# Performance work log

Hardware: AMD Instinct MI355X
Metric: run time of the kernel (lower is better)

## Reference

```python
import jax, jax.numpy as jnp
import numpy as np

N_RES = 256
D_PAIR = 128
NUM_HEADS = 16
D_HEAD = 32
D_INNER = NUM_HEADS * D_HEAD  # 512


def setup_inputs() -> dict:
    key = jax.random.key(0)
    ks = jax.random.split(key, 5)
    s_in = 1.0 / np.sqrt(D_PAIR)
    s_out = 1.0 / np.sqrt(D_INNER)
    return {
        "pair_repr": jax.random.normal(ks[0], (N_RES, N_RES, D_PAIR), jnp.float32),
        "Wq": jax.random.normal(ks[1], (D_PAIR, D_INNER), jnp.float32) * s_in,
        "bq": jnp.zeros((D_INNER,), jnp.float32),
        "Wk": jax.random.normal(ks[2], (D_PAIR, D_INNER), jnp.float32) * s_in,
        "bk": jnp.zeros((D_INNER,), jnp.float32),
        "Wv": jax.random.normal(ks[3], (D_PAIR, D_INNER), jnp.float32) * s_in,
        "bv": jnp.zeros((D_INNER,), jnp.float32),
        "Wo": jax.random.normal(ks[4], (D_INNER, D_PAIR), jnp.float32) * s_out,
        "bo": jnp.zeros((D_PAIR,), jnp.float32),
    }


def reference(pair_repr, Wq, bq, Wk, bk, Wv, bv, Wo, bo):
    N = pair_repr.shape[0]
    # Projections -> (N, N, H, Dh)
    q = (pair_repr @ Wq + bq).reshape(N, N, NUM_HEADS, D_HEAD)
    k = (pair_repr @ Wk + bk).reshape(N, N, NUM_HEADS, D_HEAD)
    v = (pair_repr @ Wv + bv).reshape(N, N, NUM_HEADS, D_HEAD)
    # Triangular attention for starting nodes: attend over k index per row i.
    a = jnp.einsum('ijhc,ikhc->ijkh', q, k) / jnp.sqrt(jnp.asarray(D_HEAD, q.dtype))
    # Lower-triangular mask over (j, k), broadcast over (i, h).
    mask = jnp.tril(jnp.ones((N, N), dtype=bool))[None, :, :, None]
    a = jnp.where(mask, a, jnp.asarray(-1e9, a.dtype))
    a = jax.nn.softmax(a, axis=2)
    o = jnp.einsum('ijkh,ikhc->ijhc', a, v).reshape(N, N, D_INNER)
    return pair_repr + (o @ Wo + bo)
```

## Files before the change

### kernel.cpp

```cpp
#include <hip/hip_runtime.h>
#include <hip/hip_bf16.h>

#define NRES 256
#define DPAIR 128
#define NHEADS 16
#define DHEAD 32
#define DINNER 512

typedef unsigned short u16;
typedef __attribute__((ext_vector_type(4))) float f32x4;
typedef __attribute__((ext_vector_type(8))) short s16x8;
typedef __attribute__((ext_vector_type(4))) short s16x4;

#define QSCALE (0.17677669529663687f * 1.4426950408889634f)

extern "C" __device__ float __ocml_native_exp2_f32(float);
__device__ __forceinline__ float fast_exp2(float x) { return __ocml_native_exp2_f32(x); }

__device__ __forceinline__ u16 f32_to_bf16(float f) {
    unsigned int u = __builtin_bit_cast(unsigned int, f);
    unsigned int r = (u + 0x7FFFu + ((u >> 16) & 1u)) >> 16;
    return (u16)r;
}

__device__ __forceinline__ unsigned pk2(float a, float b) {
    unsigned ua = __builtin_bit_cast(unsigned, a) + 0x8000u;
    unsigned ub = __builtin_bit_cast(unsigned, b) + 0x8000u;
    return __builtin_amdgcn_perm(ub, ua, 0x07060302u);
}

__device__ __forceinline__ f32x4 mfma_16x16x16_bf16(s16x4 a, s16x4 b, f32x4 c) {
#if __has_builtin(__builtin_amdgcn_mfma_f32_16x16x16bf16_1k)
    return __builtin_amdgcn_mfma_f32_16x16x16bf16_1k(a, b, c, 0, 0, 0);
#elif __has_builtin(__builtin_amdgcn_mfma_f32_16x16x16_bf16)
    return __builtin_amdgcn_mfma_f32_16x16x16_bf16(a, b, c, 0, 0, 0);
#else
    f32x4 d;
    asm volatile("v_mfma_f32_16x16x16_bf16 %0, %1, %2, %3"
                 : "=v"(d) : "v"(a), "v"(b), "v"(c));
    return d;
#endif
}

__device__ __forceinline__ void gll16(const void* g, void* l) {
    __builtin_amdgcn_global_load_lds(
        (__attribute__((address_space(1))) unsigned int*)(uintptr_t)g,
        (__attribute__((address_space(3))) unsigned int*)(unsigned int)(uintptr_t)l,
        16, 0, 0);
}

__global__ __launch_bounds__(256) void prep_all(const float* __restrict__ Wq,
                                                const float* __restrict__ Wk,
                                                const float* __restrict__ Wv,
                                                const float* __restrict__ Wo,
                                                const float* __restrict__ pair,
                                                u16* wq_t, u16* wk_t, u16* wv_t, u16* wo_t,
                                                u16* __restrict__ pairb) {
    const int b = blockIdx.x;
    if (b < 1024) {
        int id = b * 256 + threadIdx.x;
        if (id < 3 * 65536) {
            int m = id / 65536;
            int e = id % 65536;
            int k = e >> 9, n = e & 511;
            const float* W = (m == 0) ? Wq : ((m == 1) ? Wk : Wv);
            u16* Wt = (m == 0) ? wq_t : ((m == 1) ? wk_t : wv_t);
            Wt[n * 128 + k] = f32_to_bf16(W[e]);
        } else {
            int e = id - 3 * 65536;
            int k = e >> 7, n = e & 127;
            wo_t[n * 512 + k] = f32_to_bf16(Wo[e]);
        }
    } else {
        const int id = (b - 1024) * 256 + threadIdx.x;
        const float4* s = reinterpret_cast<const float4*>(pair) + (size_t)id * 2;
        const float4 v0 = s[0], v1 = s[1];
        ushort4 lo, hi;
        lo.x = f32_to_bf16(v0.x); lo.y = f32_to_bf16(v0.y);
        lo.z = f32_to_bf16(v0.z); lo.w = f32_to_bf16(v0.w);
        hi.x = f32_to_bf16(v1.x); hi.y = f32_to_bf16(v1.y);
        hi.z = f32_to_bf16(v1.z); hi.w = f32_to_bf16(v1.w);
        ushort4* d = reinterpret_cast<ushort4*>(pairb + (size_t)id * 8);
        d[0] = lo; d[1] = hi;
    }
}

__global__ __launch_bounds__(512, 4) void fused_attn(const u16* __restrict__ pairb,
                                                     const u16* __restrict__ wq_t,
                                                     const u16* __restrict__ wk_t,
                                                     const u16* __restrict__ wv_t,
                                                     const float* __restrict__ bq,
                                                     const float* __restrict__ bk,
                                                     const float* __restrict__ bv,
                                                     u16* __restrict__ o_ws) {
    __shared__ __align__(128) char ldsbuf[53760];
    u16* const wS  = (u16*)ldsbuf;
    u16* const qS  = (u16*)ldsbuf;
    u16* const vTS = (u16*)(ldsbuf + 16384);
    u16* const kS  = (u16*)(ldsbuf + 33280);

    const int bx = ((blockIdx.x & 7) << 9) | (blockIdx.x >> 3);
    const int i = bx >> 4, h = bx & 15;
    const int tid = threadIdx.x;
    const int wave = tid >> 6, lane = tid & 63;
    const int g = lane >> 4, l15 = lane & 15;
    const int j0 = wave * 32;

    for (int it = 0; it < 3; ++it) {
        const int chunk = wave * 3 + it;
        const int m = chunk >> 3;
        const int lc = chunk & 7;
        const u16* Wt = (m == 0) ? wq_t : ((m == 1) ? wk_t : wv_t);
        const int c = lc * 4 + (lane >> 4);
        const int col = (lane & 15) ^ (c & 7);
        gll16((const char*)(Wt + (size_t)(h * 32) * 128) + c * 256 + col * 16,
              (void*)(wS + (m * 32 + lc * 4) * 128));
    }
    s16x8 pf[2][4];
    {
        const u16* prow = pairb + (size_t)(i * 256 + j0 + l15) * 128;
        #pragma unroll
        for (int jf = 0; jf < 2; ++jf)
            #pragma unroll
            for (int kk = 0; kk < 4; ++kk)
                pf[jf][kk] = *reinterpret_cast<const s16x8*>(prow + jf * 16 * 128 + kk * 32 + g * 8);
    }
    __syncthreads();

    f32x4 aq[2][2], ak[2][2], av[2][2];
    {
        #pragma unroll
        for (int a = 0; a < 2; ++a)
            #pragma unroll
            for (int b = 0; b < 2; ++b) {
                aq[a][b] = f32x4{0.f, 0.f, 0.f, 0.f};
                ak[a][b] = f32x4{0.f, 0.f, 0.f, 0.f};
                av[a][b] = f32x4{0.f, 0.f, 0.f, 0.f};
            }
        #pragma unroll
        for (int kk = 0; kk < 4; ++kk) {
            s16x8 wf[3][2];
            #pragma unroll
            for (int m = 0; m < 3; ++m)
                #pragma unroll
                for (int cf = 0; cf < 2; ++cf) {
                    const int c = cf * 16 + l15;
                    const int ch = (kk * 4 + g) ^ (c & 7);
                    wf[m][cf] = *reinterpret_cast<s16x8*>(&wS[(m * 32 + c) * 128 + ch * 8]);
                }
            #pragma unroll
            for (int cf = 0; cf < 2; ++cf)
                #pragma unroll
                for (int jf = 0; jf < 2; ++jf) {
                    aq[cf][jf] = __builtin_amdgcn_mfma_f32_16x16x32_bf16(wf[0][cf], pf[jf][kk], aq[cf][jf], 0, 0, 0);
                    ak[cf][jf] = __builtin_amdgcn_mfma_f32_16x16x32_bf16(wf[1][cf], pf[jf][kk], ak[cf][jf], 0, 0, 0);
                    av[jf][cf] = __builtin_amdgcn_mfma_f32_16x16x32_bf16(pf[jf][kk], wf[2][cf], av[jf][cf], 0, 0, 0);
                }
        }
    }
    __syncthreads();

    {
        #pragma unroll
        for (int cf = 0; cf < 2; ++cf) {
            const int c = cf * 16 + g * 4;
            const float4 b4q = *reinterpret_cast<const float4*>(bq + h * 32 + c);
            const float4 b4k = *reinterpret_cast<const float4*>(bk + h * 32 + c);
            #pragma unroll
            for (int jf = 0; jf < 2; ++jf) {
                const int j = j0 + jf * 16 + l15;
                uint2 oq, ok;
                oq.x = pk2((aq[cf][jf][0] + b4q.x) * QSCALE, (aq[cf][jf][1] + b4q.y) * QSCALE);
                oq.y = pk2((aq[cf][jf][2] + b4q.z) * QSCALE, (aq[cf][jf][3] + b4q.w) * QSCALE);
                *reinterpret_cast<uint2*>(
                    &qS[j * 32 + (((cf << 1) + (g >> 1)) ^ (j & 3)) * 8 + (g & 1) * 4]) = oq;
                ok.x = pk2(ak[cf][jf][0] + b4k.x, ak[cf][jf][1] + b4k.y);
                ok.y = pk2(ak[cf][jf][2] + b4k.z, ak[cf][jf][3] + b4k.w);
                *reinterpret_cast<uint2*>(&kS[j * 40 + c]) = ok;
            }
        }
        #pragma unroll
        for (int cf = 0; cf < 2; ++cf) {
            const int c = cf * 16 + l15;
            const float bvv = bv[h * 32 + c];
            #pragma unroll
            for (int jf = 0; jf < 2; ++jf) {
                const int j = j0 + jf * 16 + g * 4;
                uint2 ov;
                ov.x = pk2(av[jf][cf][0] + bvv, av[jf][cf][1] + bvv);
                ov.y = pk2(av[jf][cf][2] + bvv, av[jf][cf][3] + bvv);
                *reinterpret_cast<uint2*>(&vTS[c * 264 + j]) = ov;
            }
        }
    }
    __syncthreads();

    const size_t obase = ((size_t)i * 256) * 512 + h * 32;
    const int tA = wave, tB = 15 - wave;

    const s16x8 qfA = *reinterpret_cast<const s16x8*>(
        &qS[(tA * 16 + l15) * 32 + (g ^ (l15 & 3)) * 8]);
    const s16x8 qfB = *reinterpret_cast<const s16x8*>(
        &qS[(tB * 16 + l15) * 32 + (g ^ (l15 & 3)) * 8]);

    const s16x4 vone = {(short)0x3F80, (short)0x3F80, (short)0x3F80, (short)0x3F80};

    f32x4 accA0 = {0.f, 0.f, 0.f, 0.f}, accA1 = {0.f, 0.f, 0.f, 0.f}, accA2 = {0.f, 0.f, 0.f, 0.f};
    f32x4 accB0 = {0.f, 0.f, 0.f, 0.f}, accB1 = {0.f, 0.f, 0.f, 0.f}, accB2 = {0.f, 0.f, 0.f, 0.f};

    auto rdK = [&](int kt) {
        return *reinterpret_cast<s16x8*>(&kS[(kt * 16 + l15) * 40 + g * 8]);
    };
    auto rdV0 = [&](int kt) {
        return *reinterpret_cast<s16x4*>(&vTS[l15 * 264 + kt * 16 + g * 4]);
    };
    auto rdV1 = [&](int kt) {
        return *reinterpret_cast<s16x4*>(&vTS[(16 + l15) * 264 + kt * 16 + g * 4]);
    };
    auto tile = [&](const s16x8& kf, const s16x4& va0, const s16x4& va1,
                    const s16x8& qf, f32x4& a0, f32x4& a1, f32x4& a2, bool dg) {
        f32x4 s = __builtin_amdgcn_mfma_f32_16x16x32_bf16(kf, qf, f32x4{0.f, 0.f, 0.f, 0.f}, 0, 0, 0);
        float p0, p1, p2, p3;
        if (dg) {
            p0 = ((g * 4 + 0) > l15) ? 0.f : fast_exp2(s[0]);
            p1 = ((g * 4 + 1) > l15) ? 0.f : fast_exp2(s[1]);
            p2 = ((g * 4 + 2) > l15) ? 0.f : fast_exp2(s[2]);
            p3 = ((g * 4 + 3) > l15) ? 0.f : fast_exp2(s[3]);
        } else {
            p0 = fast_exp2(s[0]); p1 = fast_exp2(s[1]);
            p2 = fast_exp2(s[2]); p3 = fast_exp2(s[3]);
        }
        uint2 pw;
        pw.x = pk2(p0, p1);
        pw.y = pk2(p2, p3);
        const s16x4 pb = __builtin_bit_cast(s16x4, pw);
        a0 = mfma_16x16x16_bf16(va0, pb, a0);
        a1 = mfma_16x16x16_bf16(va1, pb, a1);
        a2 = mfma_16x16x16_bf16(vone, pb, a2);
    };

    __builtin_amdgcn_s_setprio(1);
    for (int kt = 0; kt < tA; ++kt) {
        const s16x8 kf = rdK(kt);
        const s16x4 v0 = rdV0(kt), v1 = rdV1(kt);
        tile(kf, v0, v1, qfB, accB0, accB1, accB2, false);
        tile(kf, v0, v1, qfA, accA0, accA1, accA2, false);
    }
    {
        const s16x8 kf = rdK(tA);
        const s16x4 v0 = rdV0(tA), v1 = rdV1(tA);
        tile(kf, v0, v1, qfB, accB0, accB1, accB2, false);
        tile(kf, v0, v1, qfA, accA0, accA1, accA2, true);
    }
    for (int kt = tA + 1; kt < tB; ++kt) {
        const s16x8 kf = rdK(kt);
        const s16x4 v0 = rdV0(kt), v1 = rdV1(kt);
        tile(kf, v0, v1, qfB, accB0, accB1, accB2, false);
    }
    {
        const s16x8 kf = rdK(tB);
        const s16x4 v0 = rdV0(tB), v1 = rdV1(tB);
        tile(kf, v0, v1, qfB, accB0, accB1, accB2, true);
    }
    __builtin_amdgcn_s_setprio(0);

    auto store_o = [&](int jbase, const f32x4& o0, const f32x4& o1, float sum) {
        const float rinv = 1.0f / sum;
        uint2 w0, w1;
        w0.x = pk2(o0[0] * rinv, o0[1] * rinv);
        w0.y = pk2(o0[2] * rinv, o0[3] * rinv);
        w1.x = pk2(o1[0] * rinv, o1[1] * rinv);
        w1.y = pk2(o1[2] * rinv, o1[3] * rinv);
        u16* orow = o_ws + obase + (size_t)(jbase + l15) * 512;
        *reinterpret_cast<uint2*>(orow + g * 4) = w0;
        *reinterpret_cast<uint2*>(orow + 16 + g * 4) = w1;
    };
    store_o(tA * 16, accA0, accA1, accA2[0]);
    store_o(tB * 16, accB0, accB1, accB2[0]);
}

__global__ __launch_bounds__(256) void outproj(const u16* __restrict__ o_ws,
                                               const u16* __restrict__ wo_t,
                                               const float* __restrict__ pair,
                                               const float* __restrict__ bo,
                                               float* __restrict__ out) {
    __shared__ u16 As[64 * 72];
    __shared__ u16 Bs[128 * 72];
    const int tid = threadIdx.x;
    const int d = blockIdx.x;
    const int bb = ((d & 7) << 7) | (d >> 3);
    const int m0 = bb * 64;
    const int wave = tid >> 6, lane = tid & 63;
    const int g = lane >> 4, l15 = lane & 15;

    f32x4 acc[8];
    for (int c = 0; c < 8; ++c) acc[c] = f32x4{0.f, 0.f, 0.f, 0.f};

    for (int kt = 0; kt < 8; ++kt) {
        __syncthreads();
        for (int it = 0; it < 2; ++it) {
            int L = tid + it * 256;
            int row = L >> 3, seg = L & 7;
            *reinterpret_cast<s16x8*>(&As[row * 72 + seg * 8]) =
                *reinterpret_cast<const s16x8*>(o_ws + (size_t)(m0 + row) * 512 + kt * 64 + seg * 8);
        }
        for (int it = 0; it < 4; ++it) {
            int L = tid + it * 256;
            int n = L >> 3, seg = L & 7;
            *reinterpret_cast<s16x8*>(&Bs[n * 72 + seg * 8]) =
                *reinterpret_cast<const s16x8*>(wo_t + (size_t)n * 512 + kt * 64 + seg * 8);
        }
        __syncthreads();
        for (int kk = 0; kk < 2; ++kk) {
            const s16x8 a = *reinterpret_cast<s16x8*>(&As[(wave * 16 + l15) * 72 + kk * 32 + g * 8]);
            for (int c = 0; c < 8; ++c) {
                const s16x8 b = *reinterpret_cast<s16x8*>(&Bs[(c * 16 + l15) * 72 + kk * 32 + g * 8]);
                acc[c] = __builtin_amdgcn_mfma_f32_16x16x32_bf16(a, b, acc[c], 0, 0, 0);
            }
        }
    }

    for (int c = 0; c < 8; ++c) {
        const int n = c * 16 + l15;
        const float bias = bo[n];
        for (int r = 0; r < 4; ++r) {
            const size_t row = m0 + wave * 16 + g * 4 + r;
            out[row * 128 + n] = acc[c][r] + bias + pair[row * 128 + n];
        }
    }
}

extern "C" void kernel_launch(void* const* d_in, const int* in_sizes, int n_in,
                              void* d_out, int out_size, void* d_ws, size_t ws_size,
                              hipStream_t stream) {
    const float* pair = (const float*)d_in[0];
    const float* Wq = (const float*)d_in[1];
    const float* bq = (const float*)d_in[2];
    const float* Wk = (const float*)d_in[3];
    const float* bk = (const float*)d_in[4];
    const float* Wv = (const float*)d_in[5];
    const float* bv = (const float*)d_in[6];
    const float* Wo = (const float*)d_in[7];
    const float* bo = (const float*)d_in[8];
    float* out = (float*)d_out;

    char* ws = (char*)d_ws;
    u16* o_ws  = (u16*)(ws);
    u16* wq_t  = (u16*)(ws + 67108864);
    u16* wk_t  = wq_t + 65536;
    u16* wv_t  = wk_t + 65536;
    u16* wo_t  = wv_t + 65536;
    u16* pairb = (u16*)(ws + 67108864 + 1048576);

    prep_all<<<5120, 256, 0, stream>>>(Wq, Wk, Wv, Wo, pair,
                                       wq_t, wk_t, wv_t, wo_t, pairb);
    fused_attn<<<4096, 512, 0, stream>>>(pairb, wq_t, wk_t, wv_t, bq, bk, bv, o_ws);
    outproj<<<1024, 256, 0, stream>>>(o_ws, wo_t, pair, bo, out);
}
```

Baseline: 114.9 us.

## Fuse pair bf16 conversion into attention and widen PV MFMA to 32-k blocks

The separate pre-pass that converted the fp32 pair tensor to bf16 in workspace is removed. The attention kernel now loads fp32 rows directly and packs them to bf16 in registers, which avoids one full write and re-read of the pair tensor. The attention inner loop now handles 32-key blocks, so the PV and row-sum products use 16x16x32 MFMAs instead of 16x16x16. To match the new MFMA operand layout, K rows are stored in a permuted slot order. In exchange, each attention block reads twice as many bytes of pair data, and the diagonal masking now works at 32-key granularity.

New measurement: 130.4 us. 1.14x slower.

```diff
diff --git a/kernel.cpp b/kernel.cpp
--- a/kernel.cpp
+++ b/kernel.cpp
@@ -29,19 +29,6 @@
     return __builtin_amdgcn_perm(ub, ua, 0x07060302u);
 }
 
-__device__ __forceinline__ f32x4 mfma_16x16x16_bf16(s16x4 a, s16x4 b, f32x4 c) {
-#if __has_builtin(__builtin_amdgcn_mfma_f32_16x16x16bf16_1k)
-    return __builtin_amdgcn_mfma_f32_16x16x16bf16_1k(a, b, c, 0, 0, 0);
-#elif __has_builtin(__builtin_amdgcn_mfma_f32_16x16x16_bf16)
-    return __builtin_amdgcn_mfma_f32_16x16x16_bf16(a, b, c, 0, 0, 0);
-#else
-    f32x4 d;
-    asm volatile("v_mfma_f32_16x16x16_bf16 %0, %1, %2, %3"
-                 : "=v"(d) : "v"(a), "v"(b), "v"(c));
-    return d;
-#endif
-}
-
 __device__ __forceinline__ void gll16(const void* g, void* l) {
     __builtin_amdgcn_global_load_lds(
         (__attribute__((address_space(1))) unsigned int*)(uintptr_t)g,
@@ -53,39 +40,23 @@
                                                 const float* __restrict__ Wk,
                                                 const float* __restrict__ Wv,
                                                 const float* __restrict__ Wo,
-                                                const float* __restrict__ pair,
-                                                u16* wq_t, u16* wk_t, u16* wv_t, u16* wo_t,
-                                                u16* __restrict__ pairb) {
-    const int b = blockIdx.x;
-    if (b < 1024) {
-        int id = b * 256 + threadIdx.x;
-        if (id < 3 * 65536) {
-            int m = id / 65536;
-            int e = id % 65536;
-            int k = e >> 9, n = e & 511;
-            const float* W = (m == 0) ? Wq : ((m == 1) ? Wk : Wv);
-            u16* Wt = (m == 0) ? wq_t : ((m == 1) ? wk_t : wv_t);
-            Wt[n * 128 + k] = f32_to_bf16(W[e]);
-        } else {
-            int e = id - 3 * 65536;
-            int k = e >> 7, n = e & 127;
-            wo_t[n * 512 + k] = f32_to_bf16(Wo[e]);
-        }
+                                                u16* wq_t, u16* wk_t, u16* wv_t, u16* wo_t) {
+    int id = blockIdx.x * 256 + threadIdx.x;
+    if (id < 3 * 65536) {
+        int m = id / 65536;
+        int e = id % 65536;
+        int k = e >> 9, n = e & 511;
+        const float* W = (m == 0) ? Wq : ((m == 1) ? Wk : Wv);
+        u16* Wt = (m == 0) ? wq_t : ((m == 1) ? wk_t : wv_t);
+        Wt[n * 128 + k] = f32_to_bf16(W[e]);
     } else {
-        const int id = (b - 1024) * 256 + threadIdx.x;
-        const float4* s = reinterpret_cast<const float4*>(pair) + (size_t)id * 2;
-        const float4 v0 = s[0], v1 = s[1];
-        ushort4 lo, hi;
-        lo.x = f32_to_bf16(v0.x); lo.y = f32_to_bf16(v0.y);
-        lo.z = f32_to_bf16(v0.z); lo.w = f32_to_bf16(v0.w);
-        hi.x = f32_to_bf16(v1.x); hi.y = f32_to_bf16(v1.y);
-        hi.z = f32_to_bf16(v1.z); hi.w = f32_to_bf16(v1.w);
-        ushort4* d = reinterpret_cast<ushort4*>(pairb + (size_t)id * 8);
-        d[0] = lo; d[1] = hi;
-    }
-}
-
-__global__ __launch_bounds__(512, 4) void fused_attn(const u16* __restrict__ pairb,
+        int e = id - 3 * 65536;
+        int k = e >> 7, n = e & 127;
+        wo_t[n * 512 + k] = f32_to_bf16(Wo[e]);
+    }
+}
+
+__global__ __launch_bounds__(512, 4) void fused_attn(const float* __restrict__ pair,
                                                      const u16* __restrict__ wq_t,
                                                      const u16* __restrict__ wk_t,
                                                      const u16* __restrict__ wv_t,
@@ -118,12 +89,19 @@
     }
     s16x8 pf[2][4];
     {
-        const u16* prow = pairb + (size_t)(i * 256 + j0 + l15) * 128;
+        const float* prow = pair + (size_t)(i * 256 + j0 + l15) * 128;
         #pragma unroll
         for (int jf = 0; jf < 2; ++jf)
             #pragma unroll
-            for (int kk = 0; kk < 4; ++kk)
-                pf[jf][kk] = *reinterpret_cast<const s16x8*>(prow + jf * 16 * 128 + kk * 32 + g * 8);
+            for (int kk = 0; kk < 4; ++kk) {
+                const float* src = prow + jf * 16 * 128 + kk * 32 + g * 8;
+                const float4 x = *reinterpret_cast<const float4*>(src);
+                const float4 y = *reinterpret_cast<const float4*>(src + 4);
+                uint4 u4;
+                u4.x = pk2(x.x, x.y); u4.y = pk2(x.z, x.w);
+                u4.z = pk2(y.x, y.y); u4.w = pk2(y.z, y.w);
+                pf[jf][kk] = __builtin_bit_cast(s16x8, u4);
+            }
     }
     __syncthreads();
 
@@ -174,9 +152,11 @@
                 oq.y = pk2((aq[cf][jf][2] + b4q.z) * QSCALE, (aq[cf][jf][3] + b4q.w) * QSCALE);
                 *reinterpret_cast<uint2*>(
                     &qS[j * 32 + (((cf << 1) + (g >> 1)) ^ (j & 3)) * 8 + (g & 1) * 4]) = oq;
+                const int u = jf * 16 + l15;
+                const int slot = j0 + (((u & 4) << 2) | ((u & 24) >> 1) | (u & 3));
                 ok.x = pk2(ak[cf][jf][0] + b4k.x, ak[cf][jf][1] + b4k.y);
                 ok.y = pk2(ak[cf][jf][2] + b4k.z, ak[cf][jf][3] + b4k.w);
-                *reinterpret_cast<uint2*>(&kS[j * 40 + c]) = ok;
+                *reinterpret_cast<uint2*>(&kS[slot * 40 + c]) = ok;
             }
         }
         #pragma unroll
@@ -197,70 +177,76 @@
 
     const size_t obase = ((size_t)i * 256) * 512 + h * 32;
     const int tA = wave, tB = 15 - wave;
+    const int mA = tA >> 1, mB = tB >> 1;
+    const int djA = ((tA & 1) << 4) | l15;
+    const int djB = ((tB & 1) << 4) | l15;
 
     const s16x8 qfA = *reinterpret_cast<const s16x8*>(
         &qS[(tA * 16 + l15) * 32 + (g ^ (l15 & 3)) * 8]);
     const s16x8 qfB = *reinterpret_cast<const s16x8*>(
         &qS[(tB * 16 + l15) * 32 + (g ^ (l15 & 3)) * 8]);
 
-    const s16x4 vone = {(short)0x3F80, (short)0x3F80, (short)0x3F80, (short)0x3F80};
-
-    f32x4 accA0 = {0.f, 0.f, 0.f, 0.f}, accA1 = {0.f, 0.f, 0.f, 0.f}, accA2 = {0.f, 0.f, 0.f, 0.f};
-    f32x4 accB0 = {0.f, 0.f, 0.f, 0.f}, accB1 = {0.f, 0.f, 0.f, 0.f}, accB2 = {0.f, 0.f, 0.f, 0.f};
-
-    auto rdK = [&](int kt) {
-        return *reinterpret_cast<s16x8*>(&kS[(kt * 16 + l15) * 40 + g * 8]);
+    const short one = (short)0x3F80;
+    const s16x8 vones8 = {one, one, one, one, one, one, one, one};
+    const f32x4 fz = {0.f, 0.f, 0.f, 0.f};
+
+    f32x4 accA0 = fz, accA1 = fz, accA2 = fz;
+    f32x4 accB0 = fz, accB1 = fz, accB2 = fz;
+
+    s16x8 kf0, kf1, va0, va1;
+    auto rd4 = [&](int m) {
+        kf0 = *reinterpret_cast<s16x8*>(&kS[(m * 32 + l15) * 40 + g * 8]);
+        kf1 = *reinterpret_cast<s16x8*>(&kS[(m * 32 + 16 + l15) * 40 + g * 8]);
+        va0 = *reinterpret_cast<s16x8*>(&vTS[l15 * 264 + m * 32 + g * 8]);
+        va1 = *reinterpret_cast<s16x8*>(&vTS[(16 + l15) * 264 + m * 32 + g * 8]);
     };
-    auto rdV0 = [&](int kt) {
-        return *reinterpret_cast<s16x4*>(&vTS[l15 * 264 + kt * 16 + g * 4]);
+    auto blk = [&](const s16x8& qf, f32x4& a0, f32x4& a1, f32x4& a2, int dj, bool dg) {
+        f32x4 s0 = __builtin_amdgcn_mfma_f32_16x16x32_bf16(kf0, qf, fz, 0, 0, 0);
+        f32x4 s1 = __builtin_amdgcn_mfma_f32_16x16x32_bf16(kf1, qf, fz, 0, 0, 0);
+        float p0, p1, p2, p3, p4, p5, p6, p7;
+        if (dg) {
+            const int kb = 8 * g;
+            p0 = (kb + 0 > dj) ? 0.f : fast_exp2(s0[0]);
+            p1 = (kb + 1 > dj) ? 0.f : fast_exp2(s0[1]);
+            p2 = (kb + 2 > dj) ? 0.f : fast_exp2(s0[2]);
+            p3 = (kb + 3 > dj) ? 0.f : fast_exp2(s0[3]);
+            p4 = (kb + 4 > dj) ? 0.f : fast_exp2(s1[0]);
+            p5 = (kb + 5 > dj) ? 0.f : fast_exp2(s1[1]);
+            p6 = (kb + 6 > dj) ? 0.f : fast_exp2(s1[2]);
+            p7 = (kb + 7 > dj) ? 0.f : fast_exp2(s1[3]);
+        } else {
+            p0 = fast_exp2(s0[0]); p1 = fast_exp2(s0[1]);
+            p2 = fast_exp2(s0[2]); p3 = fast_exp2(s0[3]);
+            p4 = fast_exp2(s1[0]); p5 = fast_exp2(s1[1]);
+            p6 = fast_exp2(s1[2]); p7 = fast_exp2(s1[3]);
+        }
+        uint4 pw;
+        pw.x = pk2(p0, p1); pw.y = pk2(p2, p3);
+        pw.z = pk2(p4, p5); pw.w = pk2(p6, p7);
+        const s16x8 pb = __builtin_bit_cast(s16x8, pw);
+        a0 = __builtin_amdgcn_mfma_f32_16x16x32_bf16(va0, pb, a0, 0, 0, 0);
+        a1 = __builtin_amdgcn_mfma_f32_16x16x32_bf16(va1, pb, a1, 0, 0, 0);
+        a2 = __builtin_amdgcn_mfma_f32_16x16x32_bf16(vones8, pb, a2, 0, 0, 0);
     };
-    auto rdV1 = [&](int kt) {
-        return *reinterpret_cast<s16x4*>(&vTS[(16 + l15) * 264 + kt * 16 + g * 4]);
-    };
-    auto tile = [&](const s16x8& kf, const s16x4& va0, const s16x4& va1,
-                    const s16x8& qf, f32x4& a0, f32x4& a1, f32x4& a2, bool dg) {
-        f32x4 s = __builtin_amdgcn_mfma_f32_16x16x32_bf16(kf, qf, f32x4{0.f, 0.f, 0.f, 0.f}, 0, 0, 0);
-        float p0, p1, p2, p3;
-        if (dg) {
-            p0 = ((g * 4 + 0) > l15) ? 0.f : fast_exp2(s[0]);
-            p1 = ((g * 4 + 1) > l15) ? 0.f : fast_exp2(s[1]);
-            p2 = ((g * 4 + 2) > l15) ? 0.f : fast_exp2(s[2]);
-            p3 = ((g * 4 + 3) > l15) ? 0.f : fast_exp2(s[3]);
-        } else {
-            p0 = fast_exp2(s[0]); p1 = fast_exp2(s[1]);
-            p2 = fast_exp2(s[2]); p3 = fast_exp2(s[3]);
-        }
-        uint2 pw;
-        pw.x = pk2(p0, p1);
-        pw.y = pk2(p2, p3);
-        const s16x4 pb = __builtin_bit_cast(s16x4, pw);
-        a0 = mfma_16x16x16_bf16(va0, pb, a0);
-        a1 = mfma_16x16x16_bf16(va1, pb, a1);
-        a2 = mfma_16x16x16_bf16(vone, pb, a2);
-    };
 
     __builtin_amdgcn_s_setprio(1);
-    for (int kt = 0; kt < tA; ++kt) {
-        const s16x8 kf = rdK(kt);
-        const s16x4 v0 = rdV0(kt), v1 = rdV1(kt);
-        tile(kf, v0, v1, qfB, accB0, accB1, accB2, false);
-        tile(kf, v0, v1, qfA, accA0, accA1, accA2, false);
-    }
-    {
-        const s16x8 kf = rdK(tA);
-        const s16x4 v0 = rdV0(tA), v1 = rdV1(tA);
-        tile(kf, v0, v1, qfB, accB0, accB1, accB2, false);
-        tile(kf, v0, v1, qfA, accA0, accA1, accA2, true);
-    }
-    for (int kt = tA + 1; kt < tB; ++kt) {
-        const s16x8 kf = rdK(kt);
-        const s16x4 v0 = rdV0(kt), v1 = rdV1(kt);
-        tile(kf, v0, v1, qfB, accB0, accB1, accB2, false);
-    }
-    {
-        const s16x8 kf = rdK(tB);
-        const s16x4 v0 = rdV0(tB), v1 = rdV1(tB);
-        tile(kf, v0, v1, qfB, accB0, accB1, accB2, true);
+    for (int m = 0; m < mA; ++m) {
+        rd4(m);
+        blk(qfB, accB0, accB1, accB2, 0, false);
+        blk(qfA, accA0, accA1, accA2, 0, false);
+    }
+    {
+        rd4(mA);
+        blk(qfB, accB0, accB1, accB2, 0, false);
+        blk(qfA, accA0, accA1, accA2, djA, true);
+    }
+    for (int m = mA + 1; m < mB; ++m) {
+        rd4(m);
+        blk(qfB, accB0, accB1, accB2, 0, false);
+    }
+    {
+        rd4(mB);
+        blk(qfB, accB0, accB1, accB2, djB, true);
     }
     __builtin_amdgcn_s_setprio(0);
 
@@ -350,10 +336,8 @@
     u16* wk_t  = wq_t + 65536;
     u16* wv_t  = wk_t + 65536;
     u16* wo_t  = wv_t + 65536;
-    u16* pairb = (u16*)(ws + 67108864 + 1048576);
-
-    prep_all<<<5120, 256, 0, stream>>>(Wq, Wk, Wv, Wo, pair,
-                                       wq_t, wk_t, wv_t, wo_t, pairb);
-    fused_attn<<<4096, 512, 0, stream>>>(pairb, wq_t, wk_t, wv_t, bq, bk, bv, o_ws);
+
+    prep_all<<<1024, 256, 0, stream>>>(Wq, Wk, Wv, Wo, wq_t, wk_t, wv_t, wo_t);
+    fused_attn<<<4096, 512, 0, stream>>>(pair, wq_t, wk_t, wv_t, bq, bk, bv, o_ws);
     outproj<<<1024, 256, 0, stream>>>(o_ws, wo_t, pair, bo, out);
 }
```
